# Optimization experiments

Measured on AMD Instinct MI355X. Metric: run time of the kernel, lower is better.

Reference implementation:

```python
import jax, jax.numpy as jnp
import numpy as np

N_NODES = 50000
HID = 64
EPS = 1e-5
POS_COLS = np.array([0, 1, 14])  # pos_x, pos_y, battery


def setup_inputs() -> dict:
    key = jax.random.key(0)
    ks = jax.random.split(key, 10)
    x = jax.random.normal(ks[0], (N_NODES, 16), dtype=jnp.float32)
    edge_index = jax.random.randint(ks[1], (2, 1600000), 0, N_NODES, dtype=jnp.int64)
    # 6 structurally identical conv layers: Linear(6,64) -> ReLU -> Linear(64,64)
    W1 = jax.random.normal(ks[2], (6, 6, HID), dtype=jnp.float32) * (1.0 / np.sqrt(6))
    b1 = jax.random.normal(ks[3], (6, HID), dtype=jnp.float32) * 0.02
    W2 = jax.random.normal(ks[4], (6, HID, HID), dtype=jnp.float32) * (1.0 / np.sqrt(HID))
    b2 = jax.random.normal(ks[5], (6, HID), dtype=jnp.float32) * 0.02
    # 5 BatchNorm layers (training mode: batch statistics over nodes)
    bn_gamma = jnp.ones((5, HID), dtype=jnp.float32) + 0.1 * jax.random.normal(ks[6], (5, HID), dtype=jnp.float32)
    bn_beta = 0.1 * jax.random.normal(ks[7], (5, HID), dtype=jnp.float32)
    return {"x": x, "edge_index": edge_index, "W1": W1, "b1": b1,
            "W2": W2, "b2": b2, "bn_gamma": bn_gamma, "bn_beta": bn_beta}


def _conv(x, src, dst, W1, b1, W2, b2):
    # pos_battery = x[:, [0,1,14]]; message = MLP(cat(x_j - x_i, x_i)); aggr='add' at target i
    p = x[:, POS_COLS]                       # [N, 3]
    x_i = p[dst]                             # targets  [E, 3]
    x_j = p[src]                             # sources  [E, 3]
    m = jnp.concatenate([x_j - x_i, x_i], axis=1)   # [E, 6]
    h = jax.nn.relu(m @ W1 + b1) @ W2 + b2          # [E, HID]
    return jax.ops.segment_sum(h, dst, num_segments=x.shape[0])


def _bn(h, gamma, beta):
    mu = jnp.mean(h, axis=0)
    var = jnp.var(h, axis=0)  # biased, matching BatchNorm training normalization
    return (h - mu) * jax.lax.rsqrt(var + EPS) * gamma + beta


def reference(x, edge_index, W1, b1, W2, b2, bn_gamma, bn_beta):
    n = x.shape[0]
    loop = jnp.arange(n, dtype=edge_index.dtype)
    src = jnp.concatenate([edge_index[0], loop])   # add_self_loops (done per layer in torch,
    dst = jnp.concatenate([edge_index[1], loop])   # identical result every layer)
    h = x
    for l in range(6):
        h = _conv(h, src, dst, W1[l], b1[l], W2[l], b2[l])
        if l < 5:
            h = jax.nn.relu(_bn(h, bn_gamma[l], bn_beta[l]))
    return h
```

## Files before the change

kernel.cpp:

```cpp
#include <hip/hip_runtime.h>
#include <hip/hip_fp16.h>
#include <cstdint>

#define NN 50000
#define NQBLK 12500
#define NGBLK2 6250
#define EPSV 1e-5f

#define NPB 128
#define BSH 7
#define NBKT 391
#define CHUNK 4096
#define EPT 16
#define LDSE 6144

#define NSLOT 128

typedef unsigned short ushort_t;
typedef _Float16 half2v __attribute__((ext_vector_type(2)));

__global__ __launch_bounds__(256) void k_hist1(const int* __restrict__ dst, int E, int nchunk,
                                               int* __restrict__ hist, float* __restrict__ gsumsp) {
    __shared__ int cnt[NBKT];
    int t = threadIdx.x, blk = blockIdx.x;
    if (blk == 0) {
        for (int z = t; z < 5 * NSLOT * 8; z += 256) gsumsp[z] = 0.f;
    }
    for (int b = t; b < NBKT; b += 256) cnt[b] = 0;
    __syncthreads();
    int base = blk * CHUNK;
#pragma unroll
    for (int k = 0; k < EPT; ++k) {
        int e = base + k * 256 + t;
        if (e < E) atomicAdd(&cnt[dst[e] >> BSH], 1);
    }
    __syncthreads();
    for (int b = t; b < NBKT; b += 256) hist[(size_t)b * nchunk + blk] = cnt[b];
}

__global__ __launch_bounds__(256) void k_scanA(const int* __restrict__ in, int n,
                                               int* __restrict__ presum, int* __restrict__ blocksum) {
    __shared__ int lds[256];
    int t = threadIdx.x, g = blockIdx.x * 256 + t;
    int v = (g < n) ? in[g] : 0;
    lds[t] = v;
    __syncthreads();
    for (int off = 1; off < 256; off <<= 1) {
        int x = (t >= off) ? lds[t - off] : 0;
        __syncthreads();
        lds[t] += x;
        __syncthreads();
    }
    if (g < n) presum[g] = lds[t];
    if (t == 255) blocksum[blockIdx.x] = lds[255];
}

__global__ __launch_bounds__(256) void k_scanB(const int* __restrict__ blocksum,
                                               int nb, int* __restrict__ blockoff) {
    __shared__ int lds[256];
    __shared__ int carry_s;
    int t = threadIdx.x;
    if (t == 0) carry_s = 0;
    __syncthreads();
    for (int base = 0; base < nb; base += 256) {
        int g = base + t;
        int v = (g < nb) ? blocksum[g] : 0;
        lds[t] = v;
        __syncthreads();
        for (int off = 1; off < 256; off <<= 1) {
            int x = (t >= off) ? lds[t - off] : 0;
            __syncthreads();
            lds[t] += x;
            __syncthreads();
        }
        if (g < nb) blockoff[g] = lds[t] - v + carry_s;
        __syncthreads();
        if (t == 255) carry_s += lds[255];
        __syncthreads();
    }
}

__global__ __launch_bounds__(256) void k_scanC(const int* __restrict__ presum,
                                               const int* __restrict__ hist,
                                               const int* __restrict__ blockoff,
                                               int n, int nchunk, int* __restrict__ offsT) {
    int g = blockIdx.x * 256 + threadIdx.x;
    if (g < n) {
        int val = presum[g] - hist[g] + blockoff[blockIdx.x];
        int b = g / nchunk;
        int c = g - b * nchunk;
        offsT[(size_t)c * NBKT + b] = val;
    }
}

__global__ __launch_bounds__(256) void k_scatter1(const int* __restrict__ src,
                                                  const int* __restrict__ dst, int E,
                                                  const int* __restrict__ offsT,
                                                  int* __restrict__ ebuf) {
    __shared__ int pos[NBKT];
    int t = threadIdx.x, blk = blockIdx.x;
    for (int b = t; b < NBKT; b += 256) pos[b] = offsT[(size_t)blk * NBKT + b];
    __syncthreads();
    int base = blk * CHUNK;
#pragma unroll
    for (int k = 0; k < EPT; ++k) {
        int e = base + k * 256 + t;
        if (e < E) {
            int d = dst[e];
            int b = d >> BSH;
            int p = atomicAdd(&pos[b], 1);
            ebuf[p] = ((d & (NPB - 1)) << 16) | src[e];
        }
    }
}

__global__ __launch_bounds__(256) void k_bucket_csr(const int* __restrict__ ebuf,
                                                    const int* __restrict__ offsT, int E,
                                                    int* __restrict__ rowstart,
                                                    ushort_t* __restrict__ colsrc) {
    __shared__ int cnt[NPB];
    __shared__ int s[NPB];
    __shared__ int pos2[NPB];
    __shared__ ushort_t lout[LDSE];
    int t = threadIdx.x, b = blockIdx.x;
    int bstart = offsT[b];
    int bend = (b + 1 < NBKT) ? offsT[b + 1] : E;
    int m = bend - bstart;
    if (t < NPB) cnt[t] = 0;
    __syncthreads();
    for (int i = bstart + t; i < bend; i += 256) atomicAdd(&cnt[ebuf[i] >> 16], 1);
    __syncthreads();
    if (t < NPB) s[t] = cnt[t];
    __syncthreads();
    for (int off = 1; off < NPB; off <<= 1) {
        int x = (t < NPB && t >= off) ? s[t - off] : 0;
        __syncthreads();
        if (t < NPB) s[t] += x;
        __syncthreads();
    }
    if (t < NPB) {
        int excl = s[t] - cnt[t];
        int node = b * NPB + t;
        if (node < NN) rowstart[node] = bstart + excl;
        pos2[t] = excl;
    }
    __syncthreads();
    if (m <= LDSE) {
        for (int i = bstart + t; i < bend; i += 256) {
            int v = ebuf[i];
            int p = atomicAdd(&pos2[v >> 16], 1);
            lout[p] = (ushort_t)(v & 0xFFFF);
        }
        __syncthreads();
        for (int i = t; i < m; i += 256) colsrc[bstart + i] = lout[i];
    } else {
        for (int i = bstart + t; i < bend; i += 256) {
            int v = ebuf[i];
            int p = atomicAdd(&pos2[v >> 16], 1);
            colsrc[bstart + p] = (ushort_t)(v & 0xFFFF);
        }
    }
    if (b == NBKT - 1 && t == 0) rowstart[NN] = E;
}

__global__ __launch_bounds__(256) void k_q(
    const float* __restrict__ pin, int pstride, int c0, int c1, int c2,
    const float* __restrict__ W1l, const float* __restrict__ b1l,
    const float* __restrict__ scale, const float* __restrict__ shift, int use_bn,
    __half* __restrict__ qs, __half* __restrict__ qd) {
    int idx = blockIdx.x * 256 + threadIdx.x;
    int v = idx >> 6, c = idx & 63;
    const float* prow = pin + (size_t)v * pstride;
    float p0 = prow[c0], p1 = prow[c1], p2 = prow[c2];
    if (use_bn) {
        p0 = fmaxf(0.f, p0 * scale[0] + shift[0]);
        p1 = fmaxf(0.f, p1 * scale[1] + shift[1]);
        p2 = fmaxf(0.f, p2 * scale[2] + shift[2]);
    }
    float w0 = W1l[0 * 64 + c], w1 = W1l[1 * 64 + c], w2 = W1l[2 * 64 + c];
    float w3 = W1l[3 * 64 + c], w4 = W1l[4 * 64 + c], w5 = W1l[5 * 64 + c];
    qs[idx] = __float2half(p0 * w0 + p1 * w1 + p2 * w2);
    qd[idx] = __float2half(p0 * (w3 - w0) + p1 * (w4 - w1) + p2 * (w5 - w2) + b1l[c]);
}

__device__ __forceinline__ half2v bitcast_h2(unsigned int u) {
    union { unsigned int u; half2v h; } cvt;
    cvt.u = u;
    return cvt.h;
}

__device__ __forceinline__ void accum8f(const char* __restrict__ qsb, unsigned int byteoff,
                                        const half2v qd2[4], float acc[8]) {
    uint4 q = *reinterpret_cast<const uint4*>(qsb + byteoff);
    unsigned int wd[4] = {q.x, q.y, q.z, q.w};
    const half2v z2 = {(_Float16)0.0f, (_Float16)0.0f};
#pragma unroll
    for (int d = 0; d < 4; ++d) {
        half2v r = bitcast_h2(wd[d]) + qd2[d];
        r = __builtin_elementwise_max(r, z2);
        acc[2 * d]     += (float)r.x;
        acc[2 * d + 1] += (float)r.y;
    }
}

__device__ __forceinline__ void chunk_math32(const uint4 q[4], const half2v qd2[4],
                                             int r, int es, float acc[8]) {
    const half2v z2 = {(_Float16)0.0f, (_Float16)0.0f};
    half2v h[4] = {z2, z2, z2, z2};
#pragma unroll
    for (int k = 0; k < 4; ++k) {
        bool ok = ((k << 3) + es) < r;
        unsigned int wd[4] = {q[k].x, q[k].y, q[k].z, q[k].w};
#pragma unroll
        for (int d = 0; d < 4; ++d) {
            half2v t = bitcast_h2(wd[d]) + qd2[d];
            t = __builtin_elementwise_max(t, z2);
            h[d] += ok ? t : z2;
        }
    }
#pragma unroll
    for (int d = 0; d < 4; ++d) {
        acc[2 * d]     += (float)h[d].x;
        acc[2 * d + 1] += (float)h[d].y;
    }
}

__device__ __forceinline__ void pair_edge_loop(const char* __restrict__ qsb,
                                               const ushort_t* __restrict__ colsrc,
                                               int iA, int e0, int iB, int e1,
                                               int lane, int es, unsigned int cg16,
                                               const half2v qd2A[4], const half2v qd2B[4],
                                               float accA[8], float accB[8]) {
    while (iA < e0 || iB < e1) {
        int remA = e0 - iA, remB = e1 - iB;
        int rA = remA > 32 ? 32 : remA;
        int rB = remB > 32 ? 32 : remB;
        int slA = (lane < rA) ? (int)colsrc[iA + lane] : 0;
        int slB = (lane < rB) ? (int)colsrc[iB + lane] : 0;
        uint4 qA[4], qB[4];
#pragma unroll
        for (int k = 0; k < 4; ++k) {
            int s = __shfl(slA, (k << 3) + es);
            qA[k] = *reinterpret_cast<const uint4*>(qsb + (((unsigned int)(s << 7)) | cg16));
        }
#pragma unroll
        for (int k = 0; k < 4; ++k) {
            int s = __shfl(slB, (k << 3) + es);
            qB[k] = *reinterpret_cast<const uint4*>(qsb + (((unsigned int)(s << 7)) | cg16));
        }
        chunk_math32(qA, qd2A, rA, es, accA);
        chunk_math32(qB, qd2B, rB, es, accB);
        iA += rA;
        iB += rB;
    }
}

__global__ __launch_bounds__(256, 4) void k_gather3(
    const __half* __restrict__ qs, const __half* __restrict__ qd,
    const int* __restrict__ rowstart, const ushort_t* __restrict__ colsrc,
    const float* __restrict__ W2l, const float* __restrict__ b2l,
    float* __restrict__ pnext, float* __restrict__ gsum_l) {
    __shared__ float w2c[3][64];
    __shared__ float b2c[3];
    __shared__ float part[4][8];
    int tid = threadIdx.x;
    if (tid < 192) {
        int cj = tid >> 6;
        int col = (cj == 0) ? 0 : ((cj == 1) ? 1 : 14);
        w2c[cj][tid & 63] = W2l[(tid & 63) * 64 + col];
    }
    if (tid < 3) b2c[tid] = b2l[(tid == 0) ? 0 : ((tid == 1) ? 1 : 14)];
    __syncthreads();

    int w = tid >> 6, lane = tid & 63;
    int es = lane >> 3, cg = lane & 7;
    unsigned int cg16 = (unsigned int)(cg << 4);
    int v0 = (blockIdx.x * 4 + w) * 2;
    const char* qsb = (const char*)qs;

    uint4 qqA = ((const uint4*)qd)[(size_t)v0 * 8 + cg];
    uint4 qqB = ((const uint4*)qd)[(size_t)(v0 + 1) * 8 + cg];
    half2v qd2A[4], qd2B[4];
    {
        unsigned int qa[4] = {qqA.x, qqA.y, qqA.z, qqA.w};
        unsigned int qb[4] = {qqB.x, qqB.y, qqB.z, qqB.w};
#pragma unroll
        for (int d = 0; d < 4; ++d) { qd2A[d] = bitcast_h2(qa[d]); qd2B[d] = bitcast_h2(qb[d]); }
    }

    float accA[8] = {0, 0, 0, 0, 0, 0, 0, 0};
    float accB[8] = {0, 0, 0, 0, 0, 0, 0, 0};
    int s0 = rowstart[v0], e0 = rowstart[v0 + 1], e1 = rowstart[v0 + 2];
    if (es == 0) {
        accum8f(qsb, ((unsigned int)(v0 << 7)) | cg16, qd2A, accA);
        accum8f(qsb, ((unsigned int)((v0 + 1) << 7)) | cg16, qd2B, accB);
    }
    pair_edge_loop(qsb, colsrc, s0, e0, e0, e1, lane, es, cg16, qd2A, qd2B, accA, accB);

    float degA = (float)(e0 - s0 + 1);
    float degB = (float)(e1 - e0 + 1);
#pragma unroll
    for (int j = 0; j < 3; ++j) {
        float tA = 0.f, tB = 0.f;
#pragma unroll
        for (int k = 0; k < 8; ++k) {
            float wv = w2c[j][cg * 8 + k];
            tA += accA[k] * wv;
            tB += accB[k] * wv;
        }
        tA += __shfl_xor(tA, 1);  tB += __shfl_xor(tB, 1);
        tA += __shfl_xor(tA, 2);  tB += __shfl_xor(tB, 2);
        tA += __shfl_xor(tA, 4);  tB += __shfl_xor(tB, 4);
        tA += __shfl_xor(tA, 8);  tB += __shfl_xor(tB, 8);
        tA += __shfl_xor(tA, 16); tB += __shfl_xor(tB, 16);
        tA += __shfl_xor(tA, 32); tB += __shfl_xor(tB, 32);
        if (lane == 0) {
            float valA = tA + degA * b2c[j];
            float valB = tB + degB * b2c[j];
            pnext[v0 * 3 + j] = valA;
            pnext[(v0 + 1) * 3 + j] = valB;
            part[w][j] = valA + valB;
            part[w][3 + j] = valA * valA + valB * valB;
        }
    }
    __syncthreads();
    if (tid < 6) {
        float ssum = part[0][tid] + part[1][tid] + part[2][tid] + part[3][tid];
        atomicAdd(&gsum_l[(blockIdx.x & (NSLOT - 1)) * 8 + tid], ssum);
    }
}

__global__ void k_bnfin(const float* __restrict__ gs,
                        const float* __restrict__ gamma_l, const float* __restrict__ beta_l,
                        float* __restrict__ scale, float* __restrict__ shift) {
    __shared__ float red[6][8];
    __shared__ float tot[6];
    int t = threadIdx.x;
    int j = t >> 3, k = t & 7;
    if (j < 6) {
        float s = 0.f;
        for (int slot = k; slot < NSLOT; slot += 8) s += gs[slot * 8 + j];
        red[j][k] = s;
    }
    __syncthreads();
    if (t < 6) {
        float s = 0.f;
#pragma unroll
        for (int k2 = 0; k2 < 8; ++k2) s += red[t][k2];
        tot[t] = s;
    }
    __syncthreads();
    if (t < 3) {
        const int cols[3] = {0, 1, 14};
        float mu = tot[t] / (float)NN;
        float var = tot[t + 3] / (float)NN - mu * mu;
        float rs = rsqrtf(var + EPSV);
        float g = gamma_l[cols[t]];
        scale[t] = rs * g;
        shift[t] = beta_l[cols[t]] - mu * rs * g;
    }
}

__global__ __launch_bounds__(256, 4) void k_gather_full(
    const __half* __restrict__ qs, const __half* __restrict__ qd,
    const int* __restrict__ rowstart, const ushort_t* __restrict__ colsrc,
    const float* __restrict__ W2l, const float* __restrict__ b2l,
    float* __restrict__ out) {
    __shared__ float lds[4][2][64];
    int tid = threadIdx.x;
    int w = tid >> 6, lane = tid & 63;
    int es = lane >> 3, cg = lane & 7;
    unsigned int cg16 = (unsigned int)(cg << 4);
    int v0 = (blockIdx.x * 4 + w) * 2;
    const char* qsb = (const char*)qs;

    uint4 qqA = ((const uint4*)qd)[(size_t)v0 * 8 + cg];
    uint4 qqB = ((const uint4*)qd)[(size_t)(v0 + 1) * 8 + cg];
    half2v qd2A[4], qd2B[4];
    {
        unsigned int qa[4] = {qqA.x, qqA.y, qqA.z, qqA.w};
        unsigned int qb[4] = {qqB.x, qqB.y, qqB.z, qqB.w};
#pragma unroll
        for (int d = 0; d < 4; ++d) { qd2A[d] = bitcast_h2(qa[d]); qd2B[d] = bitcast_h2(qb[d]); }
    }

    float accA[8] = {0, 0, 0, 0, 0, 0, 0, 0};
    float accB[8] = {0, 0, 0, 0, 0, 0, 0, 0};
    int s0 = rowstart[v0], e0 = rowstart[v0 + 1], e1 = rowstart[v0 + 2];
    if (es == 0) {
        accum8f(qsb, ((unsigned int)(v0 << 7)) | cg16, qd2A, accA);
        accum8f(qsb, ((unsigned int)((v0 + 1) << 7)) | cg16, qd2B, accB);
    }
    pair_edge_loop(qsb, colsrc, s0, e0, e0, e1, lane, es, cg16, qd2A, qd2B, accA, accB);

#pragma unroll
    for (int k = 0; k < 8; ++k) {
        accA[k] += __shfl_xor(accA[k], 8);
        accA[k] += __shfl_xor(accA[k], 16);
        accA[k] += __shfl_xor(accA[k], 32);
        accB[k] += __shfl_xor(accB[k], 8);
        accB[k] += __shfl_xor(accB[k], 16);
        accB[k] += __shfl_xor(accB[k], 32);
    }
    if (es == 0) {
#pragma unroll
        for (int k = 0; k < 8; ++k) {
            lds[w][0][cg * 8 + k] = accA[k];
            lds[w][1][cg * 8 + k] = accB[k];
        }
    }
    __syncthreads();
    float degA = (float)(e0 - s0 + 1);
    float degB = (float)(e1 - e0 + 1);
    float bl = b2l[lane];
    float sumA = degA * bl;
    float sumB = degB * bl;
    for (int k = 0; k < 64; ++k) {
        float wv = W2l[k * 64 + lane];
        sumA += lds[w][0][k] * wv;
        sumB += lds[w][1][k] * wv;
    }
    out[(size_t)v0 * 64 + lane] = sumA;
    out[(size_t)(v0 + 1) * 64 + lane] = sumB;
}


static inline size_t align_up(size_t x) { return (x + 255) & ~(size_t)255; }

extern "C" void kernel_launch(void* const* d_in, const int* in_sizes, int n_in,
                              void* d_out, int out_size, void* d_ws, size_t ws_size,
                              hipStream_t stream) {
    const float* x     = (const float*)d_in[0];
    const int*   ei    = (const int*)d_in[1];
    const float* W1    = (const float*)d_in[2];
    const float* b1    = (const float*)d_in[3];
    const float* W2    = (const float*)d_in[4];
    const float* b2    = (const float*)d_in[5];
    const float* gamma = (const float*)d_in[6];
    const float* beta  = (const float*)d_in[7];
    float* out = (float*)d_out;
    const int E = in_sizes[1] / 2;
    const int* src = ei;
    const int* dst = ei + E;

    const int nchunk = (E + CHUNK - 1) / CHUNK;
    const int nscan  = NBKT * nchunk;
    const int nsb    = (nscan + 255) / 256;

    char* base = (char*)d_ws;
    size_t off = 0;
    __half* qs = (__half*)(base + off);     off = align_up(off + (size_t)NN * 64 * 2);
    __half* qd = (__half*)(base + off);     off = align_up(off + (size_t)NN * 64 * 2);
    float* pA = (float*)(base + off);       off = align_up(off + (size_t)NN * 3 * 4);
    float* pB = (float*)(base + off);       off = align_up(off + (size_t)NN * 3 * 4);
    int* rowstart = (int*)(base + off);     off = align_up(off + (size_t)(NN + 1) * 4);
    ushort_t* colsrc = (ushort_t*)(base + off); off = align_up(off + (size_t)E * 2);
    int* ebuf     = (int*)(base + off);     off = align_up(off + (size_t)E * 4);
    int* hist     = (int*)(base + off);     off = align_up(off + (size_t)nscan * 4);
    int* offsT    = (int*)(base + off);     off = align_up(off + (size_t)nscan * 4);
    int* presum   = (int*)(base + off);     off = align_up(off + (size_t)nscan * 4);
    int* bsum     = (int*)(base + off);     off = align_up(off + (size_t)nsb * 4);
    int* boff     = (int*)(base + off);     off = align_up(off + (size_t)nsb * 4);
    float* gsumsp = (float*)(base + off);   off = align_up(off + (size_t)5 * NSLOT * 8 * 4);
    float* scale  = (float*)(base + off);   off = align_up(off + 64 * 4);
    float* shift  = (float*)(base + off);   off = align_up(off + 64 * 4);
    (void)ws_size; (void)n_in; (void)out_size;

    k_hist1<<<nchunk, 256, 0, stream>>>(dst, E, nchunk, hist, gsumsp);
    k_scanA<<<nsb, 256, 0, stream>>>(hist, nscan, presum, bsum);
    k_scanB<<<1, 256, 0, stream>>>(bsum, nsb, boff);
    k_scanC<<<nsb, 256, 0, stream>>>(presum, hist, boff, nscan, nchunk, offsT);
    k_scatter1<<<nchunk, 256, 0, stream>>>(src, dst, E, offsT, ebuf);
    k_bucket_csr<<<NBKT, 256, 0, stream>>>(ebuf, offsT, E, rowstart, colsrc);

    float* pc = pA;
    float* pn = pB;
    for (int l = 0; l < 6; ++l) {
        const float* pin = (l == 0) ? x : pc;
        int pstride = (l == 0) ? 16 : 3;
        int c0 = 0, c1 = 1, c2 = (l == 0) ? 14 : 2;
        k_q<<<NQBLK, 256, 0, stream>>>(pin, pstride, c0, c1, c2,
                                       W1 + (size_t)l * 6 * 64, b1 + (size_t)l * 64,
                                       scale, shift, (l > 0) ? 1 : 0, qs, qd);
        if (l < 5) {
            k_gather3<<<NGBLK2, 256, 0, stream>>>(qs, qd, rowstart, colsrc,
                                                  W2 + (size_t)l * 64 * 64, b2 + (size_t)l * 64,
                                                  pn, gsumsp + (size_t)l * NSLOT * 8);
            k_bnfin<<<1, 64, 0, stream>>>(gsumsp + (size_t)l * NSLOT * 8,
                                          gamma + (size_t)l * 64, beta + (size_t)l * 64,
                                          scale, shift);
            float* tmp = pc; pc = pn; pn = tmp;
        } else {
            k_gather_full<<<NGBLK2, 256, 0, stream>>>(qs, qd, rowstart, colsrc,
                                                      W2 + (size_t)5 * 64 * 64, b2 + (size_t)5 * 64,
                                                      out);
        }
    }
}
```

Before: 436.8 us.

## Fold scanB and bnfin kernels into neighbors, vectorize k_q, prefetch edge indices

Removes the single-block k_scanB launch by having each k_scanC block reduce its own prefix of block sums. Removes the k_bnfin launch per layer by recomputing BN scale/shift inside every k_q block from the slot partial sums. Rewrites k_q so each thread produces 8 channels and writes packed uint4 half vectors, cutting threads and store count. Software-pipelines the edge index loads in pair_edge_loop so the next chunk's colsrc reads overlap the current chunk's math, at the cost of redundant per-block reductions and extra registers.

```diff
diff --git a/kernel.cpp b/kernel.cpp
--- a/kernel.cpp
+++ b/kernel.cpp
@@ -3,7 +3,7 @@
 #include <cstdint>
 
 #define NN 50000
-#define NQBLK 12500
+#define NQBLK8 1563
 #define NGBLK2 6250
 #define EPSV 1e-5f
 
@@ -55,38 +55,24 @@
     if (t == 255) blocksum[blockIdx.x] = lds[255];
 }
 
-__global__ __launch_bounds__(256) void k_scanB(const int* __restrict__ blocksum,
-                                               int nb, int* __restrict__ blockoff) {
-    __shared__ int lds[256];
-    __shared__ int carry_s;
-    int t = threadIdx.x;
-    if (t == 0) carry_s = 0;
-    __syncthreads();
-    for (int base = 0; base < nb; base += 256) {
-        int g = base + t;
-        int v = (g < nb) ? blocksum[g] : 0;
-        lds[t] = v;
-        __syncthreads();
-        for (int off = 1; off < 256; off <<= 1) {
-            int x = (t >= off) ? lds[t - off] : 0;
-            __syncthreads();
-            lds[t] += x;
-            __syncthreads();
-        }
-        if (g < nb) blockoff[g] = lds[t] - v + carry_s;
-        __syncthreads();
-        if (t == 255) carry_s += lds[255];
-        __syncthreads();
-    }
-}
-
 __global__ __launch_bounds__(256) void k_scanC(const int* __restrict__ presum,
                                                const int* __restrict__ hist,
-                                               const int* __restrict__ blockoff,
+                                               const int* __restrict__ blocksum,
                                                int n, int nchunk, int* __restrict__ offsT) {
-    int g = blockIdx.x * 256 + threadIdx.x;
+    __shared__ int lds[256];
+    int t = threadIdx.x, myblk = blockIdx.x;
+    int acc = 0;
+    for (int i = t; i < myblk; i += 256) acc += blocksum[i];
+    lds[t] = acc;
+    __syncthreads();
+    for (int off = 128; off > 0; off >>= 1) {
+        if (t < off) lds[t] += lds[t + off];
+        __syncthreads();
+    }
+    int boff = lds[0];
+    int g = myblk * 256 + t;
     if (g < n) {
-        int val = presum[g] - hist[g] + blockoff[blockIdx.x];
+        int val = presum[g] - hist[g] + boff;
         int b = g / nchunk;
         int c = g - b * nchunk;
         offsT[(size_t)c * NBKT + b] = val;
@@ -166,21 +152,66 @@
 __global__ __launch_bounds__(256) void k_q(
     const float* __restrict__ pin, int pstride, int c0, int c1, int c2,
     const float* __restrict__ W1l, const float* __restrict__ b1l,
-    const float* __restrict__ scale, const float* __restrict__ shift, int use_bn,
+    const float* __restrict__ gsum_prev, const float* __restrict__ gamma_l,
+    const float* __restrict__ beta_l, int use_bn,
     __half* __restrict__ qs, __half* __restrict__ qd) {
-    int idx = blockIdx.x * 256 + threadIdx.x;
-    int v = idx >> 6, c = idx & 63;
+    __shared__ float red[6][8];
+    __shared__ float scv[3], shv[3];
+    int tid = threadIdx.x;
+    if (use_bn) {
+        if (tid < 48) {
+            int j = tid >> 3, k = tid & 7;
+            float s = 0.f;
+            for (int slot = k; slot < NSLOT; slot += 8) s += gsum_prev[slot * 8 + j];
+            red[j][k] = s;
+        }
+        __syncthreads();
+        if (tid < 3) {
+            const int cols[3] = {0, 1, 14};
+            float sum = 0.f, sumsq = 0.f;
+#pragma unroll
+            for (int k2 = 0; k2 < 8; ++k2) { sum += red[tid][k2]; sumsq += red[tid + 3][k2]; }
+            float mu = sum / (float)NN;
+            float var = sumsq / (float)NN - mu * mu;
+            float rs = rsqrtf(var + EPSV);
+            float g = gamma_l[cols[tid]];
+            scv[tid] = rs * g;
+            shv[tid] = beta_l[cols[tid]] - mu * rs * g;
+        }
+        __syncthreads();
+    }
+    int idx = blockIdx.x * 256 + tid;
+    int v = idx >> 3, g = idx & 7;
+    if (v >= NN) return;
     const float* prow = pin + (size_t)v * pstride;
     float p0 = prow[c0], p1 = prow[c1], p2 = prow[c2];
     if (use_bn) {
-        p0 = fmaxf(0.f, p0 * scale[0] + shift[0]);
-        p1 = fmaxf(0.f, p1 * scale[1] + shift[1]);
-        p2 = fmaxf(0.f, p2 * scale[2] + shift[2]);
-    }
-    float w0 = W1l[0 * 64 + c], w1 = W1l[1 * 64 + c], w2 = W1l[2 * 64 + c];
-    float w3 = W1l[3 * 64 + c], w4 = W1l[4 * 64 + c], w5 = W1l[5 * 64 + c];
-    qs[idx] = __float2half(p0 * w0 + p1 * w1 + p2 * w2);
-    qd[idx] = __float2half(p0 * (w3 - w0) + p1 * (w4 - w1) + p2 * (w5 - w2) + b1l[c]);
+        p0 = fmaxf(0.f, p0 * scv[0] + shv[0]);
+        p1 = fmaxf(0.f, p1 * scv[1] + shv[1]);
+        p2 = fmaxf(0.f, p2 * scv[2] + shv[2]);
+    }
+    unsigned int us[4], ud[4];
+#pragma unroll
+    for (int pr = 0; pr < 4; ++pr) {
+        int c = (g << 3) + (pr << 1);
+        float w0a = W1l[c], w1a = W1l[64 + c], w2a = W1l[128 + c];
+        float qsa = p0 * w0a + p1 * w1a + p2 * w2a;
+        float qda = p0 * (W1l[192 + c] - w0a) + p1 * (W1l[256 + c] - w1a)
+                  + p2 * (W1l[320 + c] - w2a) + b1l[c];
+        int c1i = c + 1;
+        float w0b = W1l[c1i], w1b = W1l[64 + c1i], w2b = W1l[128 + c1i];
+        float qsb = p0 * w0b + p1 * w1b + p2 * w2b;
+        float qdb = p0 * (W1l[192 + c1i] - w0b) + p1 * (W1l[256 + c1i] - w1b)
+                  + p2 * (W1l[320 + c1i] - w2b) + b1l[c1i];
+        us[pr] = (unsigned int)__half_as_ushort(__float2half(qsa))
+               | ((unsigned int)__half_as_ushort(__float2half(qsb)) << 16);
+        ud[pr] = (unsigned int)__half_as_ushort(__float2half(qda))
+               | ((unsigned int)__half_as_ushort(__float2half(qdb)) << 16);
+    }
+    uint4 vs = {us[0], us[1], us[2], us[3]};
+    uint4 vd = {ud[0], ud[1], ud[2], ud[3]};
+    ((uint4*)qs)[(size_t)v * 8 + g] = vs;
+    ((uint4*)qd)[(size_t)v * 8 + g] = vd;
 }
 
 __device__ __forceinline__ half2v bitcast_h2(unsigned int u) {
@@ -224,6 +255,8 @@
         acc[2 * d + 1] += (float)h[d].y;
     }
 }
+
+__device__ __forceinline__ int clamp32(int x) { return x < 32 ? (x < 0 ? 0 : x) : 32; }
 
 __device__ __forceinline__ void pair_edge_loop(const char* __restrict__ qsb,
                                                const ushort_t* __restrict__ colsrc,
@@ -231,12 +264,12 @@
                                                int lane, int es, unsigned int cg16,
                                                const half2v qd2A[4], const half2v qd2B[4],
                                                float accA[8], float accB[8]) {
-    while (iA < e0 || iB < e1) {
-        int remA = e0 - iA, remB = e1 - iB;
-        int rA = remA > 32 ? 32 : remA;
-        int rB = remB > 32 ? 32 : remB;
-        int slA = (lane < rA) ? (int)colsrc[iA + lane] : 0;
-        int slB = (lane < rB) ? (int)colsrc[iB + lane] : 0;
+    int rA = clamp32(e0 - iA);
+    int rB = clamp32(e1 - iB);
+    if (rA == 0 && rB == 0) return;
+    int slA = (lane < rA) ? (int)colsrc[iA + lane] : 0;
+    int slB = (lane < rB) ? (int)colsrc[iB + lane] : 0;
+    while (true) {
         uint4 qA[4], qB[4];
 #pragma unroll
         for (int k = 0; k < 4; ++k) {
@@ -248,10 +281,19 @@
             int s = __shfl(slB, (k << 3) + es);
             qB[k] = *reinterpret_cast<const uint4*>(qsb + (((unsigned int)(s << 7)) | cg16));
         }
+        int iA2 = iA + rA, iB2 = iB + rB;
+        int rA2 = clamp32(e0 - iA2);
+        int rB2 = clamp32(e1 - iB2);
+        bool more = (rA2 > 0) || (rB2 > 0);
+        int slA2 = 0, slB2 = 0;
+        if (more) {
+            slA2 = (lane < rA2) ? (int)colsrc[iA2 + lane] : 0;
+            slB2 = (lane < rB2) ? (int)colsrc[iB2 + lane] : 0;
+        }
         chunk_math32(qA, qd2A, rA, es, accA);
         chunk_math32(qB, qd2B, rB, es, accB);
-        iA += rA;
-        iB += rB;
+        if (!more) break;
+        iA = iA2; iB = iB2; rA = rA2; rB = rB2; slA = slA2; slB = slB2;
     }
 }
 
@@ -327,37 +369,6 @@
     if (tid < 6) {
         float ssum = part[0][tid] + part[1][tid] + part[2][tid] + part[3][tid];
         atomicAdd(&gsum_l[(blockIdx.x & (NSLOT - 1)) * 8 + tid], ssum);
-    }
-}
-
-__global__ void k_bnfin(const float* __restrict__ gs,
-                        const float* __restrict__ gamma_l, const float* __restrict__ beta_l,
-                        float* __restrict__ scale, float* __restrict__ shift) {
-    __shared__ float red[6][8];
-    __shared__ float tot[6];
-    int t = threadIdx.x;
-    int j = t >> 3, k = t & 7;
-    if (j < 6) {
-        float s = 0.f;
-        for (int slot = k; slot < NSLOT; slot += 8) s += gs[slot * 8 + j];
-        red[j][k] = s;
-    }
-    __syncthreads();
-    if (t < 6) {
-        float s = 0.f;
-#pragma unroll
-        for (int k2 = 0; k2 < 8; ++k2) s += red[t][k2];
-        tot[t] = s;
-    }
-    __syncthreads();
-    if (t < 3) {
-        const int cols[3] = {0, 1, 14};
-        float mu = tot[t] / (float)NN;
-        float var = tot[t + 3] / (float)NN - mu * mu;
-        float rs = rsqrtf(var + EPSV);
-        float g = gamma_l[cols[t]];
-        scale[t] = rs * g;
-        shift[t] = beta_l[cols[t]] - mu * rs * g;
     }
 }
 
@@ -460,16 +471,12 @@
     int* offsT    = (int*)(base + off);     off = align_up(off + (size_t)nscan * 4);
     int* presum   = (int*)(base + off);     off = align_up(off + (size_t)nscan * 4);
     int* bsum     = (int*)(base + off);     off = align_up(off + (size_t)nsb * 4);
-    int* boff     = (int*)(base + off);     off = align_up(off + (size_t)nsb * 4);
     float* gsumsp = (float*)(base + off);   off = align_up(off + (size_t)5 * NSLOT * 8 * 4);
-    float* scale  = (float*)(base + off);   off = align_up(off + 64 * 4);
-    float* shift  = (float*)(base + off);   off = align_up(off + 64 * 4);
     (void)ws_size; (void)n_in; (void)out_size;
 
     k_hist1<<<nchunk, 256, 0, stream>>>(dst, E, nchunk, hist, gsumsp);
     k_scanA<<<nsb, 256, 0, stream>>>(hist, nscan, presum, bsum);
-    k_scanB<<<1, 256, 0, stream>>>(bsum, nsb, boff);
-    k_scanC<<<nsb, 256, 0, stream>>>(presum, hist, boff, nscan, nchunk, offsT);
+    k_scanC<<<nsb, 256, 0, stream>>>(presum, hist, bsum, nscan, nchunk, offsT);
     k_scatter1<<<nchunk, 256, 0, stream>>>(src, dst, E, offsT, ebuf);
     k_bucket_csr<<<NBKT, 256, 0, stream>>>(ebuf, offsT, E, rowstart, colsrc);
 
@@ -479,16 +486,17 @@
         const float* pin = (l == 0) ? x : pc;
         int pstride = (l == 0) ? 16 : 3;
         int c0 = 0, c1 = 1, c2 = (l == 0) ? 14 : 2;
-        k_q<<<NQBLK, 256, 0, stream>>>(pin, pstride, c0, c1, c2,
-                                       W1 + (size_t)l * 6 * 64, b1 + (size_t)l * 64,
-                                       scale, shift, (l > 0) ? 1 : 0, qs, qd);
+        const float* gsum_prev = (l == 0) ? gsumsp : gsumsp + (size_t)(l - 1) * NSLOT * 8;
+        const float* gamma_prev = (l == 0) ? gamma : gamma + (size_t)(l - 1) * 64;
+        const float* beta_prev  = (l == 0) ? beta  : beta  + (size_t)(l - 1) * 64;
+        k_q<<<NQBLK8, 256, 0, stream>>>(pin, pstride, c0, c1, c2,
+                                        W1 + (size_t)l * 6 * 64, b1 + (size_t)l * 64,
+                                        gsum_prev, gamma_prev, beta_prev,
+                                        (l > 0) ? 1 : 0, qs, qd);
         if (l < 5) {
             k_gather3<<<NGBLK2, 256, 0, stream>>>(qs, qd, rowstart, colsrc,
                                                   W2 + (size_t)l * 64 * 64, b2 + (size_t)l * 64,
                                                   pn, gsumsp + (size_t)l * NSLOT * 8);
-            k_bnfin<<<1, 64, 0, stream>>>(gsumsp + (size_t)l * NSLOT * 8,
-                                          gamma + (size_t)l * 64, beta + (size_t)l * 64,
-                                          scale, shift);
             float* tmp = pc; pc = pn; pn = tmp;
         } else {
             k_gather_full<<<NGBLK2, 256, 0, stream>>>(qs, qd, rowstart, colsrc,
```

Measured after the change: 404.6 us. -7.4%, faster.
